# Kernel optimization log

Measured on AMD Instinct MI355X. Metric: run time of the kernel, lower is better.

## Reference

```python
import jax, jax.numpy as jnp
import numpy as np

DIM = 128          # observed dim
LATENT = 128       # SDE state_size
HID = 128          # mu hidden width (hard-coded in source)
BROWNIAN = 2       # brownian_size
N_STEPS = 200      # Euler-Maruyama steps over t in [0, 1]
DT = 1.0 / N_STEPS


def _linear_init(key, fan_in, fan_out):
    # torch nn.Linear default: U(-1/sqrt(fan_in), 1/sqrt(fan_in))
    kw, kb = jax.random.split(key)
    bound = 1.0 / np.sqrt(fan_in)
    w = jax.random.uniform(kw, (fan_in, fan_out), jnp.float32, -bound, bound)
    b = jax.random.uniform(kb, (fan_out,), jnp.float32, -bound, bound)
    return w, b


def setup_inputs() -> dict:
    key = jax.random.key(0)
    ks = jax.random.split(key, 8)
    y = jax.random.normal(ks[0], (32768, DIM), jnp.float32)
    noise = jax.random.normal(ks[1], (N_STEPS, 32768, BROWNIAN), jnp.float32)
    enc_w, enc_b = _linear_init(ks[2], DIM, LATENT)
    mu_w1, mu_b1 = _linear_init(ks[3], LATENT, HID)
    mu_w2, mu_b2 = _linear_init(ks[4], HID, LATENT)
    sig_w, sig_b = _linear_init(ks[5], LATENT, LATENT * BROWNIAN)
    dec_w, dec_b = _linear_init(ks[6], LATENT, DIM)
    return {
        "y": y, "noise": noise,
        "enc_w": enc_w, "enc_b": enc_b,
        "mu_w1": mu_w1, "mu_b1": mu_b1, "mu_w2": mu_w2, "mu_b2": mu_b2,
        "sig_w": sig_w, "sig_b": sig_b,
        "dec_w": dec_w, "dec_b": dec_b,
    }


def reference(y, noise, enc_w, enc_b, mu_w1, mu_b1, mu_w2, mu_b2, sig_w, sig_b, dec_w, dec_b):
    B = y.shape[0]
    # encoder: Linear + exact GELU (torch nn.GELU default)
    z0 = jax.nn.gelu(y @ enc_w + enc_b, approximate=False)

    sqrt_dt = jnp.asarray(np.sqrt(DT), jnp.float32)

    def drift(z):  # f(t, y) = mu(y)
        h = jax.nn.gelu(z @ mu_w1 + mu_b1, approximate=False)
        return h @ mu_w2 + mu_b2

    def diffusion(z):  # g(t, y) -> [B, state, brownian]
        return (z @ sig_w + sig_b).reshape(B, LATENT, BROWNIAN)

    def step(z, xi):
        # Euler-Maruyama (Ito): z += f*dt + g @ dW,  dW = sqrt(dt)*xi
        dW = xi * sqrt_dt                      # [B, K]
        g = diffusion(z)                       # [B, D, K]
        z = z + drift(z) * DT + jnp.einsum("bdk,bk->bd", g, dW)
        return z, None

    zT, _ = jax.lax.scan(step, z0, noise)
    return zT @ dec_w + dec_b
```

## Files before the change

kernel.cpp:

```cpp
#include <hip/hip_runtime.h>
#include <math.h>

#define NSTEPS 200
#define NT     512
#define BR     64
#define SQDT_F 0.07071067811865475f
#define DT_F   0.005f
#define LOSCL  4096.0f
#define LOINV  2.44140625e-4f

typedef float  f32x4 __attribute__((ext_vector_type(4)));
typedef short  s16x8 __attribute__((ext_vector_type(8)));
typedef _Float16 h16x8 __attribute__((ext_vector_type(8)));
typedef unsigned short u16;
typedef unsigned short us4 __attribute__((ext_vector_type(4)));

#define ENC_OFF 0
#define W1_OFF  32768
#define W2_OFF  65536
#define WG0_OFF 98304
#define WG1_OFF 131072
#define DEC_OFF 163840
#define WPK_TOT 196608

__device__ __forceinline__ u16 f2h(float v) {
    _Float16 h = (_Float16)v;
    return __builtin_bit_cast(u16, h);
}
__device__ __forceinline__ float h2f(u16 u) {
    return (float)__builtin_bit_cast(_Float16, u);
}
__device__ __forceinline__ u16 split_hi(float v) { return f2h(v); }
__device__ __forceinline__ u16 split_lo(float v, u16 hi) {
    return f2h((v - h2f(hi)) * LOSCL);
}

__device__ __forceinline__ float gelu_fast(float x) {
    float ax = fabsf(x) * 0.70710678118654752f;
    float t  = __builtin_amdgcn_rcpf(fmaf(0.3275911f, ax, 1.0f));
    float p  = fmaf(t, 1.061405429f, -1.453152027f);
    p = fmaf(t, p, 1.421413741f);
    p = fmaf(t, p, -0.284496736f);
    p = fmaf(t, p, 0.254829592f);
    p = p * t;
    float e  = __expf(-ax * ax);
    float er = fmaf(-p, e, 1.0f);
    er = copysignf(er, x);
    return 0.5f * x * (1.0f + er);
}

__device__ __forceinline__ void mfma16(f32x4& d, s16x8 a, s16x8 b) {
    d = __builtin_amdgcn_mfma_f32_16x16x32_f16(
            __builtin_bit_cast(h16x8, a), __builtin_bit_cast(h16x8, b), d, 0, 0, 0);
}
__device__ __forceinline__ s16x8 ldf(const u16* p) {
    return *reinterpret_cast<const s16x8*>(p);
}

__device__ __forceinline__ int swz(int row) {
    return (row & 7) ^ ((row & 8) >> 2);
}

__global__ void prepack(const float* __restrict__ enc_w, const float* __restrict__ mu_w1,
                        const float* __restrict__ mu_w2, const float* __restrict__ sig_w,
                        const float* __restrict__ dec_w, u16* __restrict__ wpk)
{
    int u = blockIdx.x * 256 + threadIdx.x;
    if (u >= WPK_TOT) return;
    int mat  = u >> 15;
    int r    = u & 32767;
    int i    = r & 7;
    int lane = (r >> 3) & 63;
    int term = (r >> 9) & 1;
    int kc   = (r >> 10) & 3;
    int nt   = (r >> 12) & 7;
    int k = kc * 32 + (lane >> 4) * 8 + i;
    int n = nt * 16 + (lane & 15);
    float v;
    switch (mat) {
        case 0:  v = enc_w[k * 128 + n];         break;
        case 1:  v = mu_w1[k * 128 + n];         break;
        case 2:  v = mu_w2[k * 128 + n];         break;
        case 3:  v = sig_w[k * 256 + 2 * n];     break;
        case 4:  v = sig_w[k * 256 + 2 * n + 1]; break;
        default: v = dec_w[k * 128 + n];         break;
    }
    u16 hi = split_hi(v);
    wpk[u] = term ? split_lo(v, hi) : hi;
}

__global__ __launch_bounds__(NT) void sde_mfma(
    const float* __restrict__ y, const float* __restrict__ noise,
    const float* __restrict__ enc_b, const float* __restrict__ mu_b1,
    const float* __restrict__ mu_b2, const float* __restrict__ sig_b,
    const float* __restrict__ dec_b, const u16* __restrict__ wpk,
    float* __restrict__ out, int Btot)
{
    __shared__ __align__(16) u16 zbh[8192];
    __shared__ __align__(16) u16 zbl[8192];
    __shared__ __align__(16) u16 hbh[8192];
    __shared__ __align__(16) u16 hbl[8192];
    __shared__ float nsb[2][128];

    const int tid  = threadIdx.x;
    const int lane = tid & 63, wid = tid >> 6;
    const int ln   = lane & 15, lg = lane >> 4;
    const size_t brow = (size_t)blockIdx.x * BR;

    const int n0 = wid * 16 + ln;
    const float b10 = mu_b1[n0];
    const float b20 = mu_b2[n0];
    const float bg0 = sig_b[2 * n0];
    const float bg1 = sig_b[2 * n0 + 1];
    const int swzl = swz(ln);

    #pragma unroll
    for (int c = 0; c < 4; c++) {
        int q = c * NT + tid;
        int row = q >> 5, k4 = (q & 31) << 2;
        const float4 v = *reinterpret_cast<const float4*>(y + (brow + row) * 128 + k4);
        int idx = row * 128 + (((k4 >> 3) ^ swz(row)) << 3) + (k4 & 7);
        float vv[4] = {v.x, v.y, v.z, v.w};
        us4 hv, lv;
        #pragma unroll
        for (int e = 0; e < 4; e++) {
            u16 h = split_hi(vv[e]);
            u16 l = split_lo(vv[e], h);
            hv[e] = h; lv[e] = l;
        }
        *reinterpret_cast<us4*>(zbh + idx) = hv;
        *reinterpret_cast<us4*>(zbl + idx) = lv;
    }
    __syncthreads();

    float zr[4][4];

    {
        const float be0 = enc_b[n0];
        f32x4 a0[4], a1[4];
        #pragma unroll
        for (int mt = 0; mt < 4; mt++) {
            a0[mt] = f32x4{be0, be0, be0, be0};
            a1[mt] = f32x4{0, 0, 0, 0};
        }
        #pragma unroll
        for (int kc = 0; kc < 4; kc++) {
            int fo = (((wid << 2) | kc) << 10) + (lane << 3);
            s16x8 bh = ldf(wpk + ENC_OFF + fo);
            s16x8 bl = ldf(wpk + ENC_OFF + fo + 512);
            #pragma unroll
            for (int mt = 0; mt < 4; mt++) {
                int idx = (mt * 16 + ln) * 128 + ((((kc << 2) | lg) ^ swzl) << 3);
                s16x8 ah = ldf(zbh + idx);
                s16x8 al = ldf(zbl + idx);
                mfma16(a0[mt], ah, bh);
                mfma16(a1[mt], al, bh);
                mfma16(a1[mt], ah, bl);
            }
        }
        #pragma unroll
        for (int mt = 0; mt < 4; mt++)
            #pragma unroll
            for (int r = 0; r < 4; r++)
                zr[mt][r] = gelu_fast(fmaf(a1[mt][r], LOINV, a0[mt][r]));
    }
    __syncthreads();

    #pragma unroll
    for (int mt = 0; mt < 4; mt++)
        #pragma unroll
        for (int r = 0; r < 4; r++) {
            int m = 16 * mt + 4 * lg + r;
            int idx = m * 128 + (((n0 >> 3) ^ swz(m)) << 3) + (n0 & 7);
            u16 h = split_hi(zr[mt][r]);
            zbh[idx] = h;
            zbl[idx] = split_lo(zr[mt][r], h);
        }
    if (tid < 128) nsb[0][tid] = noise[brow * 2 + tid];
    __syncthreads();

    const u16* wq = wpk;

    for (int t = 0; t < NSTEPS; t++) {
        asm volatile("" : "+s"(wq));
        {
            int tn = (t + 1 < NSTEPS) ? (t + 1) : t;
            if (tid < 128) nsb[(t + 1) & 1][tid] = noise[((size_t)tn * Btot + brow) * 2 + tid];
        }
        {
            f32x4 a0[4], a1[4];
            #pragma unroll
            for (int mt = 0; mt < 4; mt++) {
                a0[mt] = f32x4{b10, b10, b10, b10};
                a1[mt] = f32x4{0, 0, 0, 0};
            }
            #pragma unroll
            for (int kc = 0; kc < 4; kc++) {
                int fo = (((wid << 2) | kc) << 10) + (lane << 3);
                s16x8 bh = ldf(wq + W1_OFF + fo);
                s16x8 bl = ldf(wq + W1_OFF + fo + 512);
                #pragma unroll
                for (int mt = 0; mt < 4; mt++) {
                    int idx = (mt * 16 + ln) * 128 + ((((kc << 2) | lg) ^ swzl) << 3);
                    s16x8 ah = ldf(zbh + idx);
                    s16x8 al = ldf(zbl + idx);
                    mfma16(a0[mt], ah, bh);
                    mfma16(a1[mt], al, bh);
                    mfma16(a1[mt], ah, bl);
                }
            }
            #pragma unroll
            for (int mt = 0; mt < 4; mt++)
                #pragma unroll
                for (int r = 0; r < 4; r++) {
                    float hv = gelu_fast(fmaf(a1[mt][r], LOINV, a0[mt][r]));
                    int m = 16 * mt + 4 * lg + r;
                    int idx = m * 128 + (((n0 >> 3) ^ swz(m)) << 3) + (n0 & 7);
                    u16 h = split_hi(hv);
                    hbh[idx] = h;
                    hbl[idx] = split_lo(hv, h);
                }
        }
        {
            f32x4 q0h[4], q0l[4], q1h[4], q1l[4];
            #pragma unroll
            for (int mt = 0; mt < 4; mt++) {
                q0h[mt] = f32x4{bg0, bg0, bg0, bg0}; q0l[mt] = f32x4{0, 0, 0, 0};
                q1h[mt] = f32x4{bg1, bg1, bg1, bg1}; q1l[mt] = f32x4{0, 0, 0, 0};
            }
            #pragma unroll 2
            for (int kc = 0; kc < 4; kc++) {
                int fo = (((wid << 2) | kc) << 10) + (lane << 3);
                s16x8 b0h = ldf(wq + WG0_OFF + fo);
                s16x8 b0l = ldf(wq + WG0_OFF + fo + 512);
                s16x8 b1h = ldf(wq + WG1_OFF + fo);
                s16x8 b1l = ldf(wq + WG1_OFF + fo + 512);
                #pragma unroll
                for (int mt = 0; mt < 4; mt++) {
                    int idx = (mt * 16 + ln) * 128 + ((((kc << 2) | lg) ^ swzl) << 3);
                    s16x8 ah = ldf(zbh + idx);
                    s16x8 al = ldf(zbl + idx);
                    mfma16(q0h[mt], ah, b0h);
                    mfma16(q0l[mt], al, b0h);
                    mfma16(q0l[mt], ah, b0l);
                    mfma16(q1h[mt], ah, b1h);
                    mfma16(q1l[mt], al, b1h);
                    mfma16(q1l[mt], ah, b1l);
                }
            }
            const float* np = nsb[t & 1];
            #pragma unroll
            for (int mt = 0; mt < 4; mt++)
                #pragma unroll
                for (int r = 0; r < 4; r++) {
                    int m = 16 * mt + 4 * lg + r;
                    float dw0 = np[2 * m] * SQDT_F;
                    float dw1 = np[2 * m + 1] * SQDT_F;
                    float gv0 = fmaf(q0l[mt][r], LOINV, q0h[mt][r]);
                    float gv1 = fmaf(q1l[mt][r], LOINV, q1h[mt][r]);
                    zr[mt][r] = fmaf(gv0, dw0, fmaf(gv1, dw1, zr[mt][r]));
                }
        }
        __syncthreads();

        {
            f32x4 a0[4], a1[4];
            #pragma unroll
            for (int mt = 0; mt < 4; mt++) {
                a0[mt] = f32x4{b20, b20, b20, b20};
                a1[mt] = f32x4{0, 0, 0, 0};
            }
            #pragma unroll
            for (int kc = 0; kc < 4; kc++) {
                int fo = (((wid << 2) | kc) << 10) + (lane << 3);
                s16x8 bh = ldf(wq + W2_OFF + fo);
                s16x8 bl = ldf(wq + W2_OFF + fo + 512);
                #pragma unroll
                for (int mt = 0; mt < 4; mt++) {
                    int idx = (mt * 16 + ln) * 128 + ((((kc << 2) | lg) ^ swzl) << 3);
                    s16x8 ah = ldf(hbh + idx);
                    s16x8 al = ldf(hbl + idx);
                    mfma16(a0[mt], ah, bh);
                    mfma16(a1[mt], al, bh);
                    mfma16(a1[mt], ah, bl);
                }
            }
            #pragma unroll
            for (int mt = 0; mt < 4; mt++)
                #pragma unroll
                for (int r = 0; r < 4; r++) {
                    float drift = fmaf(a1[mt][r], LOINV, a0[mt][r]);
                    float v = fmaf(drift, DT_F, zr[mt][r]);
                    zr[mt][r] = v;
                    int m = 16 * mt + 4 * lg + r;
                    int idx = m * 128 + (((n0 >> 3) ^ swz(m)) << 3) + (n0 & 7);
                    u16 h = split_hi(v);
                    zbh[idx] = h;
                    zbl[idx] = split_lo(v, h);
                }
        }
        __syncthreads();
    }

    {
        const float bd0 = dec_b[n0];
        f32x4 a0[4], a1[4];
        #pragma unroll
        for (int mt = 0; mt < 4; mt++) {
            a0[mt] = f32x4{bd0, bd0, bd0, bd0};
            a1[mt] = f32x4{0, 0, 0, 0};
        }
        #pragma unroll
        for (int kc = 0; kc < 4; kc++) {
            int fo = (((wid << 2) | kc) << 10) + (lane << 3);
            s16x8 bh = ldf(wpk + DEC_OFF + fo);
            s16x8 bl = ldf(wpk + DEC_OFF + fo + 512);
            #pragma unroll
            for (int mt = 0; mt < 4; mt++) {
                int idx = (mt * 16 + ln) * 128 + ((((kc << 2) | lg) ^ swzl) << 3);
                s16x8 ah = ldf(zbh + idx);
                s16x8 al = ldf(zbl + idx);
                mfma16(a0[mt], ah, bh);
                mfma16(a1[mt], al, bh);
                mfma16(a1[mt], ah, bl);
            }
        }
        #pragma unroll
        for (int mt = 0; mt < 4; mt++)
            #pragma unroll
            for (int r = 0; r < 4; r++) {
                int m = 16 * mt + 4 * lg + r;
                out[(brow + m) * 128 + n0] = fmaf(a1[mt][r], LOINV, a0[mt][r]);
            }
    }
}

extern "C" void kernel_launch(void* const* d_in, const int* in_sizes, int n_in,
                              void* d_out, int out_size, void* d_ws, size_t ws_size,
                              hipStream_t stream) {
    const float* y     = (const float*)d_in[0];
    const float* noise = (const float*)d_in[1];
    const float* enc_w = (const float*)d_in[2];
    const float* enc_b = (const float*)d_in[3];
    const float* mu_w1 = (const float*)d_in[4];
    const float* mu_b1 = (const float*)d_in[5];
    const float* mu_w2 = (const float*)d_in[6];
    const float* mu_b2 = (const float*)d_in[7];
    const float* sig_w = (const float*)d_in[8];
    const float* sig_b = (const float*)d_in[9];
    const float* dec_w = (const float*)d_in[10];
    const float* dec_b = (const float*)d_in[11];
    float* out = (float*)d_out;
    u16* wpk = (u16*)d_ws;

    const int Btot = in_sizes[0] / 128;
    prepack<<<(WPK_TOT + 255) / 256, 256, 0, stream>>>(enc_w, mu_w1, mu_w2, sig_w, dec_w, wpk);
    sde_mfma<<<Btot / BR, NT, 0, stream>>>(y, noise, enc_b, mu_b1, mu_b2, sig_b, dec_b,
                                           wpk, out, Btot);
}
```

Before: 2.877 ms.

## Switch SDE GEMMs from 16x16x32 to 32x32x16 MFMA with fragment-major LDS layout

Replaces the 16x16x32 f16 MFMA tiling (each wave owning 16 output columns across all 64 rows) with 32x32x16 MFMA tiles, where each of the 8 waves owns a 32x32 block. The weight prepack and LDS activation layout are reordered so each lane's A fragment sits contiguously, which drops the XOR swizzle. The aim is fewer MFMA issues and fewer LDS fragment loads per step, since each A fragment now feeds one large MFMA instead of being reloaded per 16-row tile. In exchange, each wave now streams its full K range of weights from global memory, the per-lane LDS stores use a new layout that may bank-conflict, and the loop partially unrolls.

```diff
diff --git a/kernel.cpp b/kernel.cpp
--- a/kernel.cpp
+++ b/kernel.cpp
@@ -9,7 +9,7 @@
 #define LOSCL  4096.0f
 #define LOINV  2.44140625e-4f
 
-typedef float  f32x4 __attribute__((ext_vector_type(4)));
+typedef float  f32x16 __attribute__((ext_vector_type(16)));
 typedef short  s16x8 __attribute__((ext_vector_type(8)));
 typedef _Float16 h16x8 __attribute__((ext_vector_type(8)));
 typedef unsigned short u16;
@@ -49,16 +49,12 @@
     return 0.5f * x * (1.0f + er);
 }
 
-__device__ __forceinline__ void mfma16(f32x4& d, s16x8 a, s16x8 b) {
-    d = __builtin_amdgcn_mfma_f32_16x16x32_f16(
+__device__ __forceinline__ void mfma32(f32x16& d, s16x8 a, s16x8 b) {
+    d = __builtin_amdgcn_mfma_f32_32x32x16_f16(
             __builtin_bit_cast(h16x8, a), __builtin_bit_cast(h16x8, b), d, 0, 0, 0);
 }
 __device__ __forceinline__ s16x8 ldf(const u16* p) {
     return *reinterpret_cast<const s16x8*>(p);
-}
-
-__device__ __forceinline__ int swz(int row) {
-    return (row & 7) ^ ((row & 8) >> 2);
 }
 
 __global__ void prepack(const float* __restrict__ enc_w, const float* __restrict__ mu_w1,
@@ -72,10 +68,10 @@
     int i    = r & 7;
     int lane = (r >> 3) & 63;
     int term = (r >> 9) & 1;
-    int kc   = (r >> 10) & 3;
-    int nt   = (r >> 12) & 7;
-    int k = kc * 32 + (lane >> 4) * 8 + i;
-    int n = nt * 16 + (lane & 15);
+    int kk   = (r >> 10) & 7;
+    int nt2  = (r >> 13) & 3;
+    int k = kk * 16 + (lane >> 5) * 8 + i;
+    int n = nt2 * 32 + (lane & 31);
     float v;
     switch (mat) {
         case 0:  v = enc_w[k * 128 + n];         break;
@@ -96,30 +92,34 @@
     const float* __restrict__ dec_b, const u16* __restrict__ wpk,
     float* __restrict__ out, int Btot)
 {
-    __shared__ __align__(16) u16 zbh[8192];
-    __shared__ __align__(16) u16 zbl[8192];
-    __shared__ __align__(16) u16 hbh[8192];
-    __shared__ __align__(16) u16 hbl[8192];
+    __shared__ __align__(16) u16 zfh[8192];
+    __shared__ __align__(16) u16 zfl[8192];
+    __shared__ __align__(16) u16 hfh[8192];
+    __shared__ __align__(16) u16 hfl[8192];
     __shared__ float nsb[2][128];
 
     const int tid  = threadIdx.x;
     const int lane = tid & 63, wid = tid >> 6;
-    const int ln   = lane & 15, lg = lane >> 4;
+    const int l31  = lane & 31, lg2 = lane >> 5;
+    const int rg   = wid >> 2, cw = wid & 3;
     const size_t brow = (size_t)blockIdx.x * BR;
 
-    const int n0 = wid * 16 + ln;
+    const int n0 = cw * 32 + l31;
     const float b10 = mu_b1[n0];
     const float b20 = mu_b2[n0];
     const float bg0 = sig_b[2 * n0];
     const float bg1 = sig_b[2 * n0 + 1];
-    const int swzl = swz(ln);
+
+    const int wbase = rg * 4096 + (n0 >> 4) * 512 + ((n0 >> 3) & 1) * 256 + (n0 & 7);
+    const int abase = rg * 4096 + (lane << 3);
 
     #pragma unroll
     for (int c = 0; c < 4; c++) {
         int q = c * NT + tid;
         int row = q >> 5, k4 = (q & 31) << 2;
         const float4 v = *reinterpret_cast<const float4*>(y + (brow + row) * 128 + k4);
-        int idx = row * 128 + (((k4 >> 3) ^ swz(row)) << 3) + (k4 & 7);
+        int addr = (row >> 5) * 4096 + (k4 >> 4) * 512
+                 + ((row & 31) + ((k4 >> 3) & 1) * 32) * 8 + (k4 & 7);
         float vv[4] = {v.x, v.y, v.z, v.w};
         us4 hv, lv;
         #pragma unroll
@@ -128,54 +128,42 @@
             u16 l = split_lo(vv[e], h);
             hv[e] = h; lv[e] = l;
         }
-        *reinterpret_cast<us4*>(zbh + idx) = hv;
-        *reinterpret_cast<us4*>(zbl + idx) = lv;
+        *reinterpret_cast<us4*>(zfh + addr) = hv;
+        *reinterpret_cast<us4*>(zfl + addr) = lv;
     }
     __syncthreads();
 
-    float zr[4][4];
+    float zr[16];
 
     {
         const float be0 = enc_b[n0];
-        f32x4 a0[4], a1[4];
-        #pragma unroll
-        for (int mt = 0; mt < 4; mt++) {
-            a0[mt] = f32x4{be0, be0, be0, be0};
-            a1[mt] = f32x4{0, 0, 0, 0};
-        }
-        #pragma unroll
-        for (int kc = 0; kc < 4; kc++) {
-            int fo = (((wid << 2) | kc) << 10) + (lane << 3);
+        f32x16 a0, a1;
+        #pragma unroll
+        for (int g = 0; g < 16; g++) { a0[g] = be0; a1[g] = 0.0f; }
+        #pragma unroll 2
+        for (int kk = 0; kk < 8; kk++) {
+            int ao = abase + kk * 512;
+            s16x8 ah = ldf(zfh + ao), al = ldf(zfl + ao);
+            int fo = (((cw << 3) | kk) << 10) + (lane << 3);
             s16x8 bh = ldf(wpk + ENC_OFF + fo);
             s16x8 bl = ldf(wpk + ENC_OFF + fo + 512);
-            #pragma unroll
-            for (int mt = 0; mt < 4; mt++) {
-                int idx = (mt * 16 + ln) * 128 + ((((kc << 2) | lg) ^ swzl) << 3);
-                s16x8 ah = ldf(zbh + idx);
-                s16x8 al = ldf(zbl + idx);
-                mfma16(a0[mt], ah, bh);
-                mfma16(a1[mt], al, bh);
-                mfma16(a1[mt], ah, bl);
-            }
-        }
-        #pragma unroll
-        for (int mt = 0; mt < 4; mt++)
-            #pragma unroll
-            for (int r = 0; r < 4; r++)
-                zr[mt][r] = gelu_fast(fmaf(a1[mt][r], LOINV, a0[mt][r]));
+            mfma32(a0, ah, bh);
+            mfma32(a1, al, bh);
+            mfma32(a1, ah, bl);
+        }
+        #pragma unroll
+        for (int g = 0; g < 16; g++)
+            zr[g] = gelu_fast(fmaf(a1[g], LOINV, a0[g]));
     }
     __syncthreads();
 
     #pragma unroll
-    for (int mt = 0; mt < 4; mt++)
-        #pragma unroll
-        for (int r = 0; r < 4; r++) {
-            int m = 16 * mt + 4 * lg + r;
-            int idx = m * 128 + (((n0 >> 3) ^ swz(m)) << 3) + (n0 & 7);
-            u16 h = split_hi(zr[mt][r]);
-            zbh[idx] = h;
-            zbl[idx] = split_lo(zr[mt][r], h);
-        }
+    for (int g = 0; g < 16; g++) {
+        int rl = (g & 3) + 8 * (g >> 2) + 4 * lg2;
+        u16 h = split_hi(zr[g]);
+        zfh[wbase + rl * 8] = h;
+        zfl[wbase + rl * 8] = split_lo(zr[g], h);
+    }
     if (tid < 128) nsb[0][tid] = noise[brow * 2 + tid];
     __syncthreads();
 
@@ -188,150 +176,115 @@
             if (tid < 128) nsb[(t + 1) & 1][tid] = noise[((size_t)tn * Btot + brow) * 2 + tid];
         }
         {
-            f32x4 a0[4], a1[4];
-            #pragma unroll
-            for (int mt = 0; mt < 4; mt++) {
-                a0[mt] = f32x4{b10, b10, b10, b10};
-                a1[mt] = f32x4{0, 0, 0, 0};
-            }
-            #pragma unroll
-            for (int kc = 0; kc < 4; kc++) {
-                int fo = (((wid << 2) | kc) << 10) + (lane << 3);
+            f32x16 a0, a1;
+            #pragma unroll
+            for (int g = 0; g < 16; g++) { a0[g] = b10; a1[g] = 0.0f; }
+            #pragma unroll 2
+            for (int kk = 0; kk < 8; kk++) {
+                int ao = abase + kk * 512;
+                s16x8 ah = ldf(zfh + ao), al = ldf(zfl + ao);
+                int fo = (((cw << 3) | kk) << 10) + (lane << 3);
                 s16x8 bh = ldf(wq + W1_OFF + fo);
                 s16x8 bl = ldf(wq + W1_OFF + fo + 512);
-                #pragma unroll
-                for (int mt = 0; mt < 4; mt++) {
-                    int idx = (mt * 16 + ln) * 128 + ((((kc << 2) | lg) ^ swzl) << 3);
-                    s16x8 ah = ldf(zbh + idx);
-                    s16x8 al = ldf(zbl + idx);
-                    mfma16(a0[mt], ah, bh);
-                    mfma16(a1[mt], al, bh);
-                    mfma16(a1[mt], ah, bl);
-                }
-            }
-            #pragma unroll
-            for (int mt = 0; mt < 4; mt++)
-                #pragma unroll
-                for (int r = 0; r < 4; r++) {
-                    float hv = gelu_fast(fmaf(a1[mt][r], LOINV, a0[mt][r]));
-                    int m = 16 * mt + 4 * lg + r;
-                    int idx = m * 128 + (((n0 >> 3) ^ swz(m)) << 3) + (n0 & 7);
-                    u16 h = split_hi(hv);
-                    hbh[idx] = h;
-                    hbl[idx] = split_lo(hv, h);
-                }
+                mfma32(a0, ah, bh);
+                mfma32(a1, al, bh);
+                mfma32(a1, ah, bl);
+            }
+            #pragma unroll
+            for (int g = 0; g < 16; g++) {
+                float hv = gelu_fast(fmaf(a1[g], LOINV, a0[g]));
+                int rl = (g & 3) + 8 * (g >> 2) + 4 * lg2;
+                u16 h = split_hi(hv);
+                hfh[wbase + rl * 8] = h;
+                hfl[wbase + rl * 8] = split_lo(hv, h);
+            }
         }
         {
-            f32x4 q0h[4], q0l[4], q1h[4], q1l[4];
-            #pragma unroll
-            for (int mt = 0; mt < 4; mt++) {
-                q0h[mt] = f32x4{bg0, bg0, bg0, bg0}; q0l[mt] = f32x4{0, 0, 0, 0};
-                q1h[mt] = f32x4{bg1, bg1, bg1, bg1}; q1l[mt] = f32x4{0, 0, 0, 0};
-            }
-            #pragma unroll 2
-            for (int kc = 0; kc < 4; kc++) {
-                int fo = (((wid << 2) | kc) << 10) + (lane << 3);
+            f32x16 q0h, q0l, q1h, q1l;
+            #pragma unroll
+            for (int g = 0; g < 16; g++) {
+                q0h[g] = bg0; q0l[g] = 0.0f;
+                q1h[g] = bg1; q1l[g] = 0.0f;
+            }
+            #pragma unroll 1
+            for (int kk = 0; kk < 8; kk++) {
+                int ao = abase + kk * 512;
+                s16x8 ah = ldf(zfh + ao), al = ldf(zfl + ao);
+                int fo = (((cw << 3) | kk) << 10) + (lane << 3);
                 s16x8 b0h = ldf(wq + WG0_OFF + fo);
                 s16x8 b0l = ldf(wq + WG0_OFF + fo + 512);
                 s16x8 b1h = ldf(wq + WG1_OFF + fo);
                 s16x8 b1l = ldf(wq + WG1_OFF + fo + 512);
-                #pragma unroll
-                for (int mt = 0; mt < 4; mt++) {
-                    int idx = (mt * 16 + ln) * 128 + ((((kc << 2) | lg) ^ swzl) << 3);
-                    s16x8 ah = ldf(zbh + idx);
-                    s16x8 al = ldf(zbl + idx);
-                    mfma16(q0h[mt], ah, b0h);
-                    mfma16(q0l[mt], al, b0h);
-                    mfma16(q0l[mt], ah, b0l);
-                    mfma16(q1h[mt], ah, b1h);
-                    mfma16(q1l[mt], al, b1h);
-                    mfma16(q1l[mt], ah, b1l);
-                }
+                mfma32(q0h, ah, b0h);
+                mfma32(q0l, al, b0h);
+                mfma32(q0l, ah, b0l);
+                mfma32(q1h, ah, b1h);
+                mfma32(q1l, al, b1h);
+                mfma32(q1l, ah, b1l);
             }
             const float* np = nsb[t & 1];
             #pragma unroll
-            for (int mt = 0; mt < 4; mt++)
-                #pragma unroll
-                for (int r = 0; r < 4; r++) {
-                    int m = 16 * mt + 4 * lg + r;
-                    float dw0 = np[2 * m] * SQDT_F;
-                    float dw1 = np[2 * m + 1] * SQDT_F;
-                    float gv0 = fmaf(q0l[mt][r], LOINV, q0h[mt][r]);
-                    float gv1 = fmaf(q1l[mt][r], LOINV, q1h[mt][r]);
-                    zr[mt][r] = fmaf(gv0, dw0, fmaf(gv1, dw1, zr[mt][r]));
-                }
+            for (int g = 0; g < 16; g++) {
+                int m = rg * 32 + (g & 3) + 8 * (g >> 2) + 4 * lg2;
+                float dw0 = np[2 * m] * SQDT_F;
+                float dw1 = np[2 * m + 1] * SQDT_F;
+                float gv0 = fmaf(q0l[g], LOINV, q0h[g]);
+                float gv1 = fmaf(q1l[g], LOINV, q1h[g]);
+                zr[g] = fmaf(gv0, dw0, fmaf(gv1, dw1, zr[g]));
+            }
         }
         __syncthreads();
 
         {
-            f32x4 a0[4], a1[4];
-            #pragma unroll
-            for (int mt = 0; mt < 4; mt++) {
-                a0[mt] = f32x4{b20, b20, b20, b20};
-                a1[mt] = f32x4{0, 0, 0, 0};
-            }
-            #pragma unroll
-            for (int kc = 0; kc < 4; kc++) {
-                int fo = (((wid << 2) | kc) << 10) + (lane << 3);
+            f32x16 a0, a1;
+            #pragma unroll
+            for (int g = 0; g < 16; g++) { a0[g] = b20; a1[g] = 0.0f; }
+            #pragma unroll 2
+            for (int kk = 0; kk < 8; kk++) {
+                int ao = abase + kk * 512;
+                s16x8 ah = ldf(hfh + ao), al = ldf(hfl + ao);
+                int fo = (((cw << 3) | kk) << 10) + (lane << 3);
                 s16x8 bh = ldf(wq + W2_OFF + fo);
                 s16x8 bl = ldf(wq + W2_OFF + fo + 512);
-                #pragma unroll
-                for (int mt = 0; mt < 4; mt++) {
-                    int idx = (mt * 16 + ln) * 128 + ((((kc << 2) | lg) ^ swzl) << 3);
-                    s16x8 ah = ldf(hbh + idx);
-                    s16x8 al = ldf(hbl + idx);
-                    mfma16(a0[mt], ah, bh);
-                    mfma16(a1[mt], al, bh);
-                    mfma16(a1[mt], ah, bl);
-                }
-            }
-            #pragma unroll
-            for (int mt = 0; mt < 4; mt++)
-                #pragma unroll
-                for (int r = 0; r < 4; r++) {
-                    float drift = fmaf(a1[mt][r], LOINV, a0[mt][r]);
-                    float v = fmaf(drift, DT_F, zr[mt][r]);
-                    zr[mt][r] = v;
-                    int m = 16 * mt + 4 * lg + r;
-                    int idx = m * 128 + (((n0 >> 3) ^ swz(m)) << 3) + (n0 & 7);
-                    u16 h = split_hi(v);
-                    zbh[idx] = h;
-                    zbl[idx] = split_lo(v, h);
-                }
+                mfma32(a0, ah, bh);
+                mfma32(a1, al, bh);
+                mfma32(a1, ah, bl);
+            }
+            #pragma unroll
+            for (int g = 0; g < 16; g++) {
+                float drift = fmaf(a1[g], LOINV, a0[g]);
+                float v = fmaf(drift, DT_F, zr[g]);
+                zr[g] = v;
+                int rl = (g & 3) + 8 * (g >> 2) + 4 * lg2;
+                u16 h = split_hi(v);
+                zfh[wbase + rl * 8] = h;
+                zfl[wbase + rl * 8] = split_lo(v, h);
+            }
         }
         __syncthreads();
     }
 
     {
         const float bd0 = dec_b[n0];
-        f32x4 a0[4], a1[4];
-        #pragma unroll
-        for (int mt = 0; mt < 4; mt++) {
-            a0[mt] = f32x4{bd0, bd0, bd0, bd0};
-            a1[mt] = f32x4{0, 0, 0, 0};
-        }
-        #pragma unroll
-        for (int kc = 0; kc < 4; kc++) {
-            int fo = (((wid << 2) | kc) << 10) + (lane << 3);
+        f32x16 a0, a1;
+        #pragma unroll
+        for (int g = 0; g < 16; g++) { a0[g] = bd0; a1[g] = 0.0f; }
+        #pragma unroll 2
+        for (int kk = 0; kk < 8; kk++) {
+            int ao = abase + kk * 512;
+            s16x8 ah = ldf(zfh + ao), al = ldf(zfl + ao);
+            int fo = (((cw << 3) | kk) << 10) + (lane << 3);
             s16x8 bh = ldf(wpk + DEC_OFF + fo);
             s16x8 bl = ldf(wpk + DEC_OFF + fo + 512);
-            #pragma unroll
-            for (int mt = 0; mt < 4; mt++) {
-                int idx = (mt * 16 + ln) * 128 + ((((kc << 2) | lg) ^ swzl) << 3);
-                s16x8 ah = ldf(zbh + idx);
-                s16x8 al = ldf(zbl + idx);
-                mfma16(a0[mt], ah, bh);
-                mfma16(a1[mt], al, bh);
-                mfma16(a1[mt], ah, bl);
-            }
-        }
-        #pragma unroll
-        for (int mt = 0; mt < 4; mt++)
-            #pragma unroll
-            for (int r = 0; r < 4; r++) {
-                int m = 16 * mt + 4 * lg + r;
-                out[(brow + m) * 128 + n0] = fmaf(a1[mt][r], LOINV, a0[mt][r]);
-            }
+            mfma32(a0, ah, bh);
+            mfma32(a1, al, bh);
+            mfma32(a1, ah, bl);
+        }
+        #pragma unroll
+        for (int g = 0; g < 16; g++) {
+            int m = rg * 32 + (g & 3) + 8 * (g >> 2) + 4 * lg2;
+            out[(brow + m) * 128 + n0] = fmaf(a1[g], LOINV, a0[g]);
+        }
     }
 }
 
```

Result: slower. 3.480 ms (+21.0%).

## Halve block to 32 rows, four waves each computing two N-tiles

Applied to the files above, without the earlier changes.

Shrinks the workgroup from 512 threads over 64 batch rows to 256 threads over 32 rows. Each wave now owns two 16-column output tiles across two 16-row M-tiles instead of one column tile across four M-tiles. A-fragments loaded from LDS are reused across both column tiles, and LDS use per block is halved, which doubles the block count and may allow more blocks per CU. In exchange, each wave loads twice as many weight fragments per step, and the diffusion GEMM now runs as a non-unrolled loop over the two column tiles.

```diff
diff --git a/kernel.cpp b/kernel.cpp
--- a/kernel.cpp
+++ b/kernel.cpp
@@ -2,8 +2,8 @@
 #include <math.h>
 
 #define NSTEPS 200
-#define NT     512
-#define BR     64
+#define NT     256
+#define BR     32
 #define SQDT_F 0.07071067811865475f
 #define DT_F   0.005f
 #define LOSCL  4096.0f
@@ -96,22 +96,22 @@
     const float* __restrict__ dec_b, const u16* __restrict__ wpk,
     float* __restrict__ out, int Btot)
 {
-    __shared__ __align__(16) u16 zbh[8192];
-    __shared__ __align__(16) u16 zbl[8192];
-    __shared__ __align__(16) u16 hbh[8192];
-    __shared__ __align__(16) u16 hbl[8192];
-    __shared__ float nsb[2][128];
+    __shared__ __align__(16) u16 zbh[4096];
+    __shared__ __align__(16) u16 zbl[4096];
+    __shared__ __align__(16) u16 hbh[4096];
+    __shared__ __align__(16) u16 hbl[4096];
+    __shared__ float nsb[2][64];
 
     const int tid  = threadIdx.x;
     const int lane = tid & 63, wid = tid >> 6;
     const int ln   = lane & 15, lg = lane >> 4;
     const size_t brow = (size_t)blockIdx.x * BR;
 
-    const int n0 = wid * 16 + ln;
-    const float b10 = mu_b1[n0];
-    const float b20 = mu_b2[n0];
-    const float bg0 = sig_b[2 * n0];
-    const float bg1 = sig_b[2 * n0 + 1];
+    const int n0 = wid * 32 + ln, n1 = n0 + 16;
+    const float b10 = mu_b1[n0],  b11 = mu_b1[n1];
+    const float b20 = mu_b2[n0],  b21 = mu_b2[n1];
+    const float bg00 = sig_b[2 * n0],     bg01 = sig_b[2 * n1];
+    const float bg10 = sig_b[2 * n0 + 1], bg11 = sig_b[2 * n1 + 1];
     const int swzl = swz(ln);
 
     #pragma unroll
@@ -133,50 +133,62 @@
     }
     __syncthreads();
 
-    float zr[4][4];
+    float zr[2][2][4];
 
     {
-        const float be0 = enc_b[n0];
-        f32x4 a0[4], a1[4];
-        #pragma unroll
-        for (int mt = 0; mt < 4; mt++) {
-            a0[mt] = f32x4{be0, be0, be0, be0};
-            a1[mt] = f32x4{0, 0, 0, 0};
+        const float be0 = enc_b[n0], be1 = enc_b[n1];
+        f32x4 a0[2][2], a1[2][2];
+        #pragma unroll
+        for (int mt = 0; mt < 2; mt++) {
+            a0[0][mt] = f32x4{be0, be0, be0, be0}; a1[0][mt] = f32x4{0, 0, 0, 0};
+            a0[1][mt] = f32x4{be1, be1, be1, be1}; a1[1][mt] = f32x4{0, 0, 0, 0};
         }
         #pragma unroll
         for (int kc = 0; kc < 4; kc++) {
-            int fo = (((wid << 2) | kc) << 10) + (lane << 3);
-            s16x8 bh = ldf(wpk + ENC_OFF + fo);
-            s16x8 bl = ldf(wpk + ENC_OFF + fo + 512);
-            #pragma unroll
-            for (int mt = 0; mt < 4; mt++) {
+            s16x8 ah[2], al[2];
+            #pragma unroll
+            for (int mt = 0; mt < 2; mt++) {
                 int idx = (mt * 16 + ln) * 128 + ((((kc << 2) | lg) ^ swzl) << 3);
-                s16x8 ah = ldf(zbh + idx);
-                s16x8 al = ldf(zbl + idx);
-                mfma16(a0[mt], ah, bh);
-                mfma16(a1[mt], al, bh);
-                mfma16(a1[mt], ah, bl);
-            }
-        }
-        #pragma unroll
-        for (int mt = 0; mt < 4; mt++)
-            #pragma unroll
-            for (int r = 0; r < 4; r++)
-                zr[mt][r] = gelu_fast(fmaf(a1[mt][r], LOINV, a0[mt][r]));
+                ah[mt] = ldf(zbh + idx);
+                al[mt] = ldf(zbl + idx);
+            }
+            #pragma unroll
+            for (int j = 0; j < 2; j++) {
+                int nt = wid * 2 + j;
+                int fo = (((nt << 2) | kc) << 10) + (lane << 3);
+                s16x8 bh = ldf(wpk + ENC_OFF + fo);
+                s16x8 bl = ldf(wpk + ENC_OFF + fo + 512);
+                #pragma unroll
+                for (int mt = 0; mt < 2; mt++) {
+                    mfma16(a0[j][mt], ah[mt], bh);
+                    mfma16(a1[j][mt], al[mt], bh);
+                    mfma16(a1[j][mt], ah[mt], bl);
+                }
+            }
+        }
+        #pragma unroll
+        for (int j = 0; j < 2; j++)
+            #pragma unroll
+            for (int mt = 0; mt < 2; mt++)
+                #pragma unroll
+                for (int r = 0; r < 4; r++)
+                    zr[j][mt][r] = gelu_fast(fmaf(a1[j][mt][r], LOINV, a0[j][mt][r]));
     }
     __syncthreads();
 
     #pragma unroll
-    for (int mt = 0; mt < 4; mt++)
-        #pragma unroll
-        for (int r = 0; r < 4; r++) {
-            int m = 16 * mt + 4 * lg + r;
-            int idx = m * 128 + (((n0 >> 3) ^ swz(m)) << 3) + (n0 & 7);
-            u16 h = split_hi(zr[mt][r]);
-            zbh[idx] = h;
-            zbl[idx] = split_lo(zr[mt][r], h);
-        }
-    if (tid < 128) nsb[0][tid] = noise[brow * 2 + tid];
+    for (int j = 0; j < 2; j++)
+        #pragma unroll
+        for (int mt = 0; mt < 2; mt++)
+            #pragma unroll
+            for (int r = 0; r < 4; r++) {
+                int m = 16 * mt + 4 * lg + r, n = j ? n1 : n0;
+                int idx = m * 128 + (((n >> 3) ^ swz(m)) << 3) + (n & 7);
+                u16 h = split_hi(zr[j][mt][r]);
+                zbh[idx] = h;
+                zbl[idx] = split_lo(zr[j][mt][r], h);
+            }
+    if (tid < 64) nsb[0][tid] = noise[brow * 2 + tid];
     __syncthreads();
 
     const u16* wq = wpk;
@@ -185,72 +197,90 @@
         asm volatile("" : "+s"(wq));
         {
             int tn = (t + 1 < NSTEPS) ? (t + 1) : t;
-            if (tid < 128) nsb[(t + 1) & 1][tid] = noise[((size_t)tn * Btot + brow) * 2 + tid];
+            if (tid < 64) nsb[(t + 1) & 1][tid] = noise[((size_t)tn * Btot + brow) * 2 + tid];
         }
         {
-            f32x4 a0[4], a1[4];
-            #pragma unroll
-            for (int mt = 0; mt < 4; mt++) {
-                a0[mt] = f32x4{b10, b10, b10, b10};
-                a1[mt] = f32x4{0, 0, 0, 0};
+            f32x4 a0[2][2], a1[2][2];
+            #pragma unroll
+            for (int mt = 0; mt < 2; mt++) {
+                a0[0][mt] = f32x4{b10, b10, b10, b10}; a1[0][mt] = f32x4{0, 0, 0, 0};
+                a0[1][mt] = f32x4{b11, b11, b11, b11}; a1[1][mt] = f32x4{0, 0, 0, 0};
             }
             #pragma unroll
             for (int kc = 0; kc < 4; kc++) {
-                int fo = (((wid << 2) | kc) << 10) + (lane << 3);
-                s16x8 bh = ldf(wq + W1_OFF + fo);
-                s16x8 bl = ldf(wq + W1_OFF + fo + 512);
-                #pragma unroll
-                for (int mt = 0; mt < 4; mt++) {
+                s16x8 ah[2], al[2];
+                #pragma unroll
+                for (int mt = 0; mt < 2; mt++) {
                     int idx = (mt * 16 + ln) * 128 + ((((kc << 2) | lg) ^ swzl) << 3);
-                    s16x8 ah = ldf(zbh + idx);
-                    s16x8 al = ldf(zbl + idx);
-                    mfma16(a0[mt], ah, bh);
-                    mfma16(a1[mt], al, bh);
-                    mfma16(a1[mt], ah, bl);
-                }
-            }
-            #pragma unroll
-            for (int mt = 0; mt < 4; mt++)
-                #pragma unroll
-                for (int r = 0; r < 4; r++) {
-                    float hv = gelu_fast(fmaf(a1[mt][r], LOINV, a0[mt][r]));
-                    int m = 16 * mt + 4 * lg + r;
-                    int idx = m * 128 + (((n0 >> 3) ^ swz(m)) << 3) + (n0 & 7);
-                    u16 h = split_hi(hv);
-                    hbh[idx] = h;
-                    hbl[idx] = split_lo(hv, h);
-                }
-        }
-        {
-            f32x4 q0h[4], q0l[4], q1h[4], q1l[4];
-            #pragma unroll
-            for (int mt = 0; mt < 4; mt++) {
-                q0h[mt] = f32x4{bg0, bg0, bg0, bg0}; q0l[mt] = f32x4{0, 0, 0, 0};
-                q1h[mt] = f32x4{bg1, bg1, bg1, bg1}; q1l[mt] = f32x4{0, 0, 0, 0};
-            }
+                    ah[mt] = ldf(zbh + idx);
+                    al[mt] = ldf(zbl + idx);
+                }
+                #pragma unroll
+                for (int j = 0; j < 2; j++) {
+                    int nt = wid * 2 + j;
+                    int fo = (((nt << 2) | kc) << 10) + (lane << 3);
+                    s16x8 bh = ldf(wq + W1_OFF + fo);
+                    s16x8 bl = ldf(wq + W1_OFF + fo + 512);
+                    #pragma unroll
+                    for (int mt = 0; mt < 2; mt++) {
+                        mfma16(a0[j][mt], ah[mt], bh);
+                        mfma16(a1[j][mt], al[mt], bh);
+                        mfma16(a1[j][mt], ah[mt], bl);
+                    }
+                }
+            }
+            #pragma unroll
+            for (int j = 0; j < 2; j++)
+                #pragma unroll
+                for (int mt = 0; mt < 2; mt++)
+                    #pragma unroll
+                    for (int r = 0; r < 4; r++) {
+                        float hv = gelu_fast(fmaf(a1[j][mt][r], LOINV, a0[j][mt][r]));
+                        int m = 16 * mt + 4 * lg + r, n = j ? n1 : n0;
+                        int idx = m * 128 + (((n >> 3) ^ swz(m)) << 3) + (n & 7);
+                        u16 h = split_hi(hv);
+                        hbh[idx] = h;
+                        hbl[idx] = split_lo(hv, h);
+                    }
+        }
+        const float* np = nsb[t & 1];
+        #pragma unroll 1
+        for (int j = 0; j < 2; j++) {
+            const float bgA = j ? bg01 : bg00;
+            const float bgB = j ? bg11 : bg10;
+            f32x4 q0h[2], q0l[2], q1h[2], q1l[2];
+            #pragma unroll
+            for (int mt = 0; mt < 2; mt++) {
+                q0h[mt] = f32x4{bgA, bgA, bgA, bgA}; q0l[mt] = f32x4{0, 0, 0, 0};
+                q1h[mt] = f32x4{bgB, bgB, bgB, bgB}; q1l[mt] = f32x4{0, 0, 0, 0};
+            }
+            const int nt = wid * 2 + j;
             #pragma unroll 2
             for (int kc = 0; kc < 4; kc++) {
-                int fo = (((wid << 2) | kc) << 10) + (lane << 3);
+                s16x8 ah[2], al[2];
+                #pragma unroll
+                for (int mt = 0; mt < 2; mt++) {
+                    int idx = (mt * 16 + ln) * 128 + ((((kc << 2) | lg) ^ swzl) << 3);
+                    ah[mt] = ldf(zbh + idx);
+                    al[mt] = ldf(zbl + idx);
+                }
+                int fo = (((nt << 2) | kc) << 10) + (lane << 3);
                 s16x8 b0h = ldf(wq + WG0_OFF + fo);
                 s16x8 b0l = ldf(wq + WG0_OFF + fo + 512);
                 s16x8 b1h = ldf(wq + WG1_OFF + fo);
                 s16x8 b1l = ldf(wq + WG1_OFF + fo + 512);
                 #pragma unroll
-                for (int mt = 0; mt < 4; mt++) {
-                    int idx = (mt * 16 + ln) * 128 + ((((kc << 2) | lg) ^ swzl) << 3);
-                    s16x8 ah = ldf(zbh + idx);
-                    s16x8 al = ldf(zbl + idx);
-                    mfma16(q0h[mt], ah, b0h);
-                    mfma16(q0l[mt], al, b0h);
-                    mfma16(q0l[mt], ah, b0l);
-                    mfma16(q1h[mt], ah, b1h);
-                    mfma16(q1l[mt], al, b1h);
-                    mfma16(q1l[mt], ah, b1l);
-                }
-            }
-            const float* np = nsb[t & 1];
-            #pragma unroll
-            for (int mt = 0; mt < 4; mt++)
+                for (int mt = 0; mt < 2; mt++) {
+                    mfma16(q0h[mt], ah[mt], b0h);
+                    mfma16(q0l[mt], al[mt], b0h);
+                    mfma16(q0l[mt], ah[mt], b0l);
+                    mfma16(q1h[mt], ah[mt], b1h);
+                    mfma16(q1l[mt], al[mt], b1h);
+                    mfma16(q1l[mt], ah[mt], b1l);
+                }
+            }
+            #pragma unroll
+            for (int mt = 0; mt < 2; mt++)
                 #pragma unroll
                 for (int r = 0; r < 4; r++) {
                     int m = 16 * mt + 4 * lg + r;
@@ -258,80 +288,100 @@
                     float dw1 = np[2 * m + 1] * SQDT_F;
                     float gv0 = fmaf(q0l[mt][r], LOINV, q0h[mt][r]);
                     float gv1 = fmaf(q1l[mt][r], LOINV, q1h[mt][r]);
-                    zr[mt][r] = fmaf(gv0, dw0, fmaf(gv1, dw1, zr[mt][r]));
+                    zr[j][mt][r] = fmaf(gv0, dw0, fmaf(gv1, dw1, zr[j][mt][r]));
                 }
         }
         __syncthreads();
 
         {
-            f32x4 a0[4], a1[4];
-            #pragma unroll
-            for (int mt = 0; mt < 4; mt++) {
-                a0[mt] = f32x4{b20, b20, b20, b20};
-                a1[mt] = f32x4{0, 0, 0, 0};
+            f32x4 a0[2][2], a1[2][2];
+            #pragma unroll
+            for (int mt = 0; mt < 2; mt++) {
+                a0[0][mt] = f32x4{b20, b20, b20, b20}; a1[0][mt] = f32x4{0, 0, 0, 0};
+                a0[1][mt] = f32x4{b21, b21, b21, b21}; a1[1][mt] = f32x4{0, 0, 0, 0};
             }
             #pragma unroll
             for (int kc = 0; kc < 4; kc++) {
-                int fo = (((wid << 2) | kc) << 10) + (lane << 3);
-                s16x8 bh = ldf(wq + W2_OFF + fo);
-                s16x8 bl = ldf(wq + W2_OFF + fo + 512);
-                #pragma unroll
-                for (int mt = 0; mt < 4; mt++) {
+                s16x8 ah[2], al[2];
+                #pragma unroll
+                for (int mt = 0; mt < 2; mt++) {
                     int idx = (mt * 16 + ln) * 128 + ((((kc << 2) | lg) ^ swzl) << 3);
-                    s16x8 ah = ldf(hbh + idx);
-                    s16x8 al = ldf(hbl + idx);
-                    mfma16(a0[mt], ah, bh);
-                    mfma16(a1[mt], al, bh);
-                    mfma16(a1[mt], ah, bl);
-                }
-            }
-            #pragma unroll
-            for (int mt = 0; mt < 4; mt++)
-                #pragma unroll
-                for (int r = 0; r < 4; r++) {
-                    float drift = fmaf(a1[mt][r], LOINV, a0[mt][r]);
-                    float v = fmaf(drift, DT_F, zr[mt][r]);
-                    zr[mt][r] = v;
-                    int m = 16 * mt + 4 * lg + r;
-                    int idx = m * 128 + (((n0 >> 3) ^ swz(m)) << 3) + (n0 & 7);
-                    u16 h = split_hi(v);
-                    zbh[idx] = h;
-                    zbl[idx] = split_lo(v, h);
-                }
+                    ah[mt] = ldf(hbh + idx);
+                    al[mt] = ldf(hbl + idx);
+                }
+                #pragma unroll
+                for (int j = 0; j < 2; j++) {
+                    int nt = wid * 2 + j;
+                    int fo = (((nt << 2) | kc) << 10) + (lane << 3);
+                    s16x8 bh = ldf(wq + W2_OFF + fo);
+                    s16x8 bl = ldf(wq + W2_OFF + fo + 512);
+                    #pragma unroll
+                    for (int mt = 0; mt < 2; mt++) {
+                        mfma16(a0[j][mt], ah[mt], bh);
+                        mfma16(a1[j][mt], al[mt], bh);
+                        mfma16(a1[j][mt], ah[mt], bl);
+                    }
+                }
+            }
+            #pragma unroll
+            for (int j = 0; j < 2; j++)
+                #pragma unroll
+                for (int mt = 0; mt < 2; mt++)
+                    #pragma unroll
+                    for (int r = 0; r < 4; r++) {
+                        float drift = fmaf(a1[j][mt][r], LOINV, a0[j][mt][r]);
+                        float v = fmaf(drift, DT_F, zr[j][mt][r]);
+                        zr[j][mt][r] = v;
+                        int m = 16 * mt + 4 * lg + r, n = j ? n1 : n0;
+                        int idx = m * 128 + (((n >> 3) ^ swz(m)) << 3) + (n & 7);
+                        u16 h = split_hi(v);
+                        zbh[idx] = h;
+                        zbl[idx] = split_lo(v, h);
+                    }
         }
         __syncthreads();
     }
 
     {
-        const float bd0 = dec_b[n0];
-        f32x4 a0[4], a1[4];
-        #pragma unroll
-        for (int mt = 0; mt < 4; mt++) {
-            a0[mt] = f32x4{bd0, bd0, bd0, bd0};
-            a1[mt] = f32x4{0, 0, 0, 0};
+        const float bd0 = dec_b[n0], bd1 = dec_b[n1];
+        f32x4 a0[2][2], a1[2][2];
+        #pragma unroll
+        for (int mt = 0; mt < 2; mt++) {
+            a0[0][mt] = f32x4{bd0, bd0, bd0, bd0}; a1[0][mt] = f32x4{0, 0, 0, 0};
+            a0[1][mt] = f32x4{bd1, bd1, bd1, bd1}; a1[1][mt] = f32x4{0, 0, 0, 0};
         }
         #pragma unroll
         for (int kc = 0; kc < 4; kc++) {
-            int fo = (((wid << 2) | kc) << 10) + (lane << 3);
-            s16x8 bh = ldf(wpk + DEC_OFF + fo);
-            s16x8 bl = ldf(wpk + DEC_OFF + fo + 512);
-            #pragma unroll
-            for (int mt = 0; mt < 4; mt++) {
+            s16x8 ah[2], al[2];
+            #pragma unroll
+            for (int mt = 0; mt < 2; mt++) {
                 int idx = (mt * 16 + ln) * 128 + ((((kc << 2) | lg) ^ swzl) << 3);
-                s16x8 ah = ldf(zbh + idx);
-                s16x8 al = ldf(zbl + idx);
-                mfma16(a0[mt], ah, bh);
-                mfma16(a1[mt], al, bh);
-                mfma16(a1[mt], ah, bl);
-            }
-        }
-        #pragma unroll
-        for (int mt = 0; mt < 4; mt++)
-            #pragma unroll
-            for (int r = 0; r < 4; r++) {
-                int m = 16 * mt + 4 * lg + r;
-                out[(brow + m) * 128 + n0] = fmaf(a1[mt][r], LOINV, a0[mt][r]);
-            }
+                ah[mt] = ldf(zbh + idx);
+                al[mt] = ldf(zbl + idx);
+            }
+            #pragma unroll
+            for (int j = 0; j < 2; j++) {
+                int nt = wid * 2 + j;
+                int fo = (((nt << 2) | kc) << 10) + (lane << 3);
+                s16x8 bh = ldf(wpk + DEC_OFF + fo);
+                s16x8 bl = ldf(wpk + DEC_OFF + fo + 512);
+                #pragma unroll
+                for (int mt = 0; mt < 2; mt++) {
+                    mfma16(a0[j][mt], ah[mt], bh);
+                    mfma16(a1[j][mt], al[mt], bh);
+                    mfma16(a1[j][mt], ah[mt], bl);
+                }
+            }
+        }
+        #pragma unroll
+        for (int j = 0; j < 2; j++)
+            #pragma unroll
+            for (int mt = 0; mt < 2; mt++)
+                #pragma unroll
+                for (int r = 0; r < 4; r++) {
+                    int m = 16 * mt + 4 * lg + r, n = j ? n1 : n0;
+                    out[(brow + m) * 128 + n] = fmaf(a1[j][mt][r], LOINV, a0[j][mt][r]);
+                }
     }
 }
 
```

After: 5.437 ms. 89.0% more time.
